# Kernel tuning notes

Hardware: AMD Instinct MI355X
Metric: run time of the kernel (lower is better)

Reference implementation:

```python
import jax, jax.numpy as jnp
import numpy as np

N_NODES = 100000
N_EDGES = 1600000
DIMS = [(2, 128), (128, 128), (128, 32), (32, 32), (32, 32)]


def setup_inputs() -> dict:
    key = jax.random.key(0)
    ks = jax.random.split(key, 2 + 3 * len(DIMS) + 2)
    x = jax.random.normal(ks[0], (N_NODES, 2), dtype=jnp.float32)
    edge_index = jax.random.randint(ks[1], (2, N_EDGES), 0, N_NODES, dtype=jnp.int32)
    inp = {"x": x, "edge_index": edge_index, "batch_size": 100}
    k = 2
    for i, (cin, cout) in enumerate(DIMS, start=1):
        s = 1.0 / np.sqrt(cin)
        inp[f"Wl{i}"] = jax.random.normal(ks[k], (cin, cout), dtype=jnp.float32) * s; k += 1
        inp[f"bl{i}"] = jnp.zeros((cout,), dtype=jnp.float32)
        inp[f"Wr{i}"] = jax.random.normal(ks[k], (cin, cout), dtype=jnp.float32) * s; k += 1
    inp["W_out"] = jax.random.normal(ks[k], (32, 1), dtype=jnp.float32) * (1.0 / np.sqrt(32.0)); k += 1
    inp["b_out"] = jnp.zeros((1,), dtype=jnp.float32)
    return inp


def reference(x, edge_index, batch_size,
              Wl1, bl1, Wr1, Wl2, bl2, Wr2, Wl3, bl3, Wr3,
              Wl4, bl4, Wr4, Wl5, bl5, Wr5, W_out, b_out):
    src, dst = edge_index[0], edge_index[1]
    h = x.reshape(-1, 2)
    n = h.shape[0]
    # in-degree per target node, clamped to 1 (PyG mean aggr gives 0 for isolated nodes)
    deg = jax.ops.segment_sum(jnp.ones_like(src, dtype=h.dtype), dst, num_segments=n)
    inv_deg = (1.0 / jnp.maximum(deg, 1.0))[:, None]

    def sage(h, Wl, bl, Wr):
        # mean-aggregate neighbor features, then SAGEConv: lin_l(agg) + lin_r(h)
        agg = jax.ops.segment_sum(h[src], dst, num_segments=n) * inv_deg
        return agg @ Wl + bl + h @ Wr

    for Wl, bl, Wr in ((Wl1, bl1, Wr1), (Wl2, bl2, Wr2), (Wl3, bl3, Wr3),
                       (Wl4, bl4, Wr4), (Wl5, bl5, Wr5)):
        h = jax.nn.relu(sage(h, Wl, bl, Wr))
    # dropout is identity in eval mode
    out = h @ W_out + b_out  # [n, 1]
    return out.reshape(batch_size, -1)
```

## Files before the change

### kernel.cpp

```cpp
#include <hip/hip_runtime.h>
#include <hip/hip_bf16.h>

#define N_NODES 100000
#define N_EDGES 1600000
#define NBUCK 256
#define NODES_PER_BUCKET 391
#define EDGES_PER_CHUNK (N_EDGES / NBUCK)
#define FILL_LDS_CAP 8192

typedef __bf16 bf16x8 __attribute__((ext_vector_type(8)));
typedef float f32x4 __attribute__((ext_vector_type(4)));


__device__ inline unsigned short f2bf_rne(float v) {
    unsigned u = __float_as_uint(v);
    u += 0x7fffu + ((u >> 16) & 1u);
    return (unsigned short)(u >> 16);
}

__device__ inline unsigned pack_bf(float a, float b) {
    return (unsigned)f2bf_rne(a) | ((unsigned)f2bf_rne(b) << 16);
}

__device__ inline void acc8_bf(float* a, uint4 p) {
    a[0] += __uint_as_float(p.x << 16);
    a[1] += __uint_as_float(p.x & 0xffff0000u);
    a[2] += __uint_as_float(p.y << 16);
    a[3] += __uint_as_float(p.y & 0xffff0000u);
    a[4] += __uint_as_float(p.z << 16);
    a[5] += __uint_as_float(p.z & 0xffff0000u);
    a[6] += __uint_as_float(p.w << 16);
    a[7] += __uint_as_float(p.w & 0xffff0000u);
}


__global__ __launch_bounds__(256) void pa_count(const int* __restrict__ dst,
                                                int* __restrict__ blkCntT) {
    __shared__ int hist[NBUCK];
    hist[threadIdx.x] = 0;
    __syncthreads();
    int b0 = blockIdx.x * EDGES_PER_CHUNK;
    int b1 = min(b0 + EDGES_PER_CHUNK, N_EDGES);
    for (int i = b0 + (int)threadIdx.x; i < b1; i += 256) {
        int d = __builtin_nontemporal_load(&dst[i]);
        atomicAdd(&hist[d / NODES_PER_BUCKET], 1);
    }
    __syncthreads();
    blkCntT[threadIdx.x * NBUCK + blockIdx.x] = hist[threadIdx.x];
}

__global__ __launch_bounds__(256) void pa_scan1(const int* __restrict__ blkCntT,
                                                int* __restrict__ blkBaseL,
                                                int* __restrict__ bucketTotal) {
    __shared__ int s[256];
    int t = threadIdx.x;
    int v = blkCntT[blockIdx.x * NBUCK + t];
    s[t] = v;
    __syncthreads();
    for (int off = 1; off < 256; off <<= 1) {
        int u = (t >= off) ? s[t - off] : 0;
        __syncthreads();
        s[t] += u;
        __syncthreads();
    }
    blkBaseL[blockIdx.x * NBUCK + t] = s[t] - v;
    if (t == 255) bucketTotal[blockIdx.x] = s[255];
}

__global__ __launch_bounds__(256) void pa_scan2(const int* __restrict__ bucketTotal,
                                                int* __restrict__ bstart,
                                                int* __restrict__ offsets) {
    __shared__ int s[256];
    int t = threadIdx.x;
    int v = bucketTotal[t];
    s[t] = v;
    __syncthreads();
    for (int off = 1; off < 256; off <<= 1) {
        int u = (t >= off) ? s[t - off] : 0;
        __syncthreads();
        s[t] += u;
        __syncthreads();
    }
    bstart[t] = s[t] - v;
    if (t == 255) {
        bstart[256] = s[255];
        offsets[N_NODES] = s[255];
    }
}

__global__ __launch_bounds__(256) void pa_scatter(const int* __restrict__ src,
                                                  const int* __restrict__ dst,
                                                  const int* __restrict__ blkBaseL,
                                                  const int* __restrict__ bstart,
                                                  int2* __restrict__ staging) {
    __shared__ int hist[NBUCK];
    __shared__ int runStart[NBUCK];
    __shared__ int cur[NBUCK];
    __shared__ int gbase[NBUCK];
    __shared__ int2 buf[EDGES_PER_CHUNK];

    const int tid = threadIdx.x;
    const int g = blockIdx.x;
    const int b0 = g * EDGES_PER_CHUNK;
    const int b1 = min(b0 + EDGES_PER_CHUNK, N_EDGES);

    hist[tid] = 0;
    __syncthreads();
    for (int i = b0 + tid; i < b1; i += 256) {
        int d = __builtin_nontemporal_load(&dst[i]);
        atomicAdd(&hist[d / NODES_PER_BUCKET], 1);
    }
    __syncthreads();
    {
        __shared__ int s[256];
        int v = hist[tid];
        s[tid] = v;
        __syncthreads();
        for (int off = 1; off < 256; off <<= 1) {
            int u = (tid >= off) ? s[tid - off] : 0;
            __syncthreads();
            s[tid] += u;
            __syncthreads();
        }
        runStart[tid] = s[tid] - v;
        cur[tid] = s[tid] - v;
        gbase[tid] = bstart[tid] + blkBaseL[tid * NBUCK + g];
    }
    __syncthreads();
    for (int i = b0 + tid; i < b1; i += 256) {
        int d = __builtin_nontemporal_load(&dst[i]);
        int s_ = __builtin_nontemporal_load(&src[i]);
        int k = d / NODES_PER_BUCKET;
        int p = atomicAdd(&cur[k], 1);
        buf[p] = make_int2(s_, d);
    }
    __syncthreads();
    int cnt = b1 - b0;
    for (int i = tid; i < cnt; i += 256) {
        int2 e = buf[i];
        int k = e.y / NODES_PER_BUCKET;
        staging[gbase[k] + (i - runStart[k])] = e;
    }
}

__global__ __launch_bounds__(512) void pc_fill(const int2* __restrict__ staging,
                                               const int* __restrict__ bstart,
                                               int* __restrict__ ssrc,
                                               int* __restrict__ offsets,
                                               float* __restrict__ inv_deg) {
    __shared__ int scnt[NODES_PER_BUCKET];
    __shared__ int sexc[NODES_PER_BUCKET];
    __shared__ int scur[NODES_PER_BUCKET];
    __shared__ int ssrcL[FILL_LDS_CAP];

    const int tid = threadIdx.x;
    const int b = blockIdx.x;
    const int node0 = b * NODES_PER_BUCKET;
    const int nn = min(node0 + NODES_PER_BUCKET, N_NODES) - node0;
    if (nn <= 0) return;
    const int es = bstart[b], ee = bstart[b + 1];
    const int cnt = ee - es;

    for (int j = tid; j < nn; j += 512) scnt[j] = 0;
    __syncthreads();
    for (int i = es + tid; i < ee; i += 512) {
        int2 e = staging[i];
        atomicAdd(&scnt[e.y - node0], 1);
    }
    __syncthreads();

    if (tid < 64) {
        int base = tid * 7;
        int vals[7];
        int run = 0;
#pragma unroll
        for (int j = 0; j < 7; ++j) {
            int idx = base + j;
            int c = (idx < nn) ? scnt[idx] : 0;
            vals[j] = run;
            run += c;
        }
        int inc = run;
#pragma unroll
        for (int off = 1; off < 64; off <<= 1) {
            int u = __shfl_up(inc, off, 64);
            if (tid >= off) inc += u;
        }
        int laneExcl = inc - run;
#pragma unroll
        for (int j = 0; j < 7; ++j) {
            int idx = base + j;
            if (idx < nn) sexc[idx] = laneExcl + vals[j];
        }
    }
    __syncthreads();

    for (int j = tid; j < nn; j += 512) {
        int c = scnt[j];
        int ex = sexc[j];
        offsets[node0 + j] = es + ex;
        inv_deg[node0 + j] = 1.0f / (float)max(c, 1);
        scur[j] = ex;
    }
    __syncthreads();

    if (cnt <= FILL_LDS_CAP) {
        for (int i = es + tid; i < ee; i += 512) {
            int2 e = staging[i];
            int p = atomicAdd(&scur[e.y - node0], 1);
            ssrcL[p] = e.x;
        }
        __syncthreads();
        for (int i = tid; i < cnt; i += 512) ssrc[es + i] = ssrcL[i];
    } else {
        for (int i = es + tid; i < ee; i += 512) {
            int2 e = staging[i];
            int p = atomicAdd(&scur[e.y - node0], 1);
            ssrc[es + p] = e.x;
        }
    }
}


__global__ __launch_bounds__(256) void aggregate_bf128(const unsigned short* __restrict__ hb,
                                                       const int* __restrict__ offs,
                                                       const int* __restrict__ ssrc,
                                                       const float* __restrict__ inv_deg,
                                                       unsigned short* __restrict__ aggb,
                                                       int nnodes) {
    int t = blockIdx.x * 256 + threadIdx.x;
    if (t >= nnodes * 16) return;
    int node = t >> 4;
    int c = t & 15;
    int b = offs[node], e = offs[node + 1];
    const uint4* __restrict__ hb4 = (const uint4*)hb;
    float acc[8] = {0.f, 0.f, 0.f, 0.f, 0.f, 0.f, 0.f, 0.f};
    int i = b;
    for (; i + 4 <= e; i += 4) {
        uint4 p0 = hb4[(size_t)ssrc[i] * 16 + c];
        uint4 p1 = hb4[(size_t)ssrc[i + 1] * 16 + c];
        uint4 p2 = hb4[(size_t)ssrc[i + 2] * 16 + c];
        uint4 p3 = hb4[(size_t)ssrc[i + 3] * 16 + c];
        acc8_bf(acc, p0);
        acc8_bf(acc, p1);
        acc8_bf(acc, p2);
        acc8_bf(acc, p3);
    }
    for (; i < e; ++i) {
        uint4 p = hb4[(size_t)ssrc[i] * 16 + c];
        acc8_bf(acc, p);
    }
    float s = inv_deg[node];
    uint4 o;
    o.x = pack_bf(acc[0] * s, acc[1] * s);
    o.y = pack_bf(acc[2] * s, acc[3] * s);
    o.z = pack_bf(acc[4] * s, acc[5] * s);
    o.w = pack_bf(acc[6] * s, acc[7] * s);
    ((uint4*)aggb)[t] = o;
}

__global__ __launch_bounds__(256) void aggregate_bf32(const unsigned short* __restrict__ hb,
                                                      const int* __restrict__ offs,
                                                      const int* __restrict__ ssrc,
                                                      const float* __restrict__ inv_deg,
                                                      float* __restrict__ agg, int nnodes) {
    int t = blockIdx.x * 256 + threadIdx.x;
    if (t >= nnodes * 4) return;
    int node = t >> 2;
    int c = t & 3;
    int b = offs[node], e = offs[node + 1];
    const uint4* __restrict__ hb4 = (const uint4*)hb;
    float acc[8] = {0.f, 0.f, 0.f, 0.f, 0.f, 0.f, 0.f, 0.f};
    int i = b;
    for (; i + 4 <= e; i += 4) {
        uint4 p0 = hb4[(size_t)ssrc[i] * 4 + c];
        uint4 p1 = hb4[(size_t)ssrc[i + 1] * 4 + c];
        uint4 p2 = hb4[(size_t)ssrc[i + 2] * 4 + c];
        uint4 p3 = hb4[(size_t)ssrc[i + 3] * 4 + c];
        acc8_bf(acc, p0);
        acc8_bf(acc, p1);
        acc8_bf(acc, p2);
        acc8_bf(acc, p3);
    }
    for (; i < e; ++i) {
        uint4 p = hb4[(size_t)ssrc[i] * 4 + c];
        acc8_bf(acc, p);
    }
    float s = inv_deg[node];
    float4* outp = (float4*)&agg[(size_t)node * 32 + c * 8];
    outp[0] = make_float4(acc[0] * s, acc[1] * s, acc[2] * s, acc[3] * s);
    outp[1] = make_float4(acc[4] * s, acc[5] * s, acc[6] * s, acc[7] * s);
}

__global__ __launch_bounds__(256) void aggregate2(const float* __restrict__ h,
                                                  const int* __restrict__ offs,
                                                  const int* __restrict__ ssrc,
                                                  const float* __restrict__ inv_deg,
                                                  float* __restrict__ agg, int nnodes) {
    int node = blockIdx.x * blockDim.x + threadIdx.x;
    if (node >= nnodes) return;
    int b = offs[node], e = offs[node + 1];
    const float2* __restrict__ h2 = (const float2*)h;
    float2 a0 = make_float2(0.f, 0.f), a1 = make_float2(0.f, 0.f);
    int i = b;
    for (; i + 2 <= e; i += 2) {
        float2 v = h2[ssrc[i]];
        float2 w = h2[ssrc[i + 1]];
        a0.x += v.x; a0.y += v.y;
        a1.x += w.x; a1.y += w.y;
    }
    if (i < e) {
        float2 v = h2[ssrc[i]];
        a0.x += v.x; a0.y += v.y;
    }
    float s = inv_deg[node];
    ((float2*)agg)[node] = make_float2((a0.x + a1.x) * s, (a0.y + a1.y) * s);
}


__global__ __launch_bounds__(256) void prep_wt(const float* __restrict__ Wl,
                                               const float* __restrict__ Wr,
                                               unsigned short* __restrict__ Wt) {
    int idx = blockIdx.x * 256 + threadIdx.x;
    int n = idx >> 8;
    int k = idx & 255;
    float v = (k < 128) ? Wl[k * 128 + n] : Wr[(k - 128) * 128 + n];
    Wt[idx] = f2bf_rne(v);
}

__global__ __launch_bounds__(256) void prep_w3(const float* __restrict__ Wl3,
                                               const float* __restrict__ Wr3,
                                               unsigned short* __restrict__ W3c) {
    int idx = blockIdx.x * 256 + threadIdx.x;
    if (idx >= 64 * 128) return;
    int n = idx >> 7;
    int k = idx & 127;
    float v = (n < 32) ? Wl3[k * 32 + n] : Wr3[k * 32 + (n - 32)];
    W3c[idx] = f2bf_rne(v);
}


__global__ __launch_bounds__(256) void gemm_l2_mfma(const unsigned short* __restrict__ Ab,
                                                    const unsigned short* __restrict__ Hb,
                                                    const unsigned short* __restrict__ Wt,
                                                    const float* __restrict__ bias,
                                                    const unsigned short* __restrict__ W3c,
                                                    unsigned short* __restrict__ g3b,
                                                    float* __restrict__ p3, int M) {
    constexpr int BM = 128, BK = 64;
    __shared__ unsigned short smem[26112];
#define SA(r, c) smem[(r) * 72 + (c)]
#define SB(r, c) smem[9216 + (r) * 72 + (c)]
#define SH(r, c) smem[(r) * 136 + (c)]
#define SW3(r, c) smem[17408 + (r) * 136 + (c)]

    const int tid = threadIdx.x;
    const int m0 = blockIdx.x * BM;
    const int lane = tid & 63;
    const int wid = tid >> 6;
    const int l15 = lane & 15;
    const int quad = lane >> 4;
    const int wm = (wid >> 1) * 64;
    const int wn = (wid & 1) * 64;

    f32x4 acc[4][4];
#pragma unroll
    for (int i = 0; i < 4; ++i)
#pragma unroll
        for (int j = 0; j < 4; ++j) acc[i][j] = (f32x4){0.f, 0.f, 0.f, 0.f};

    for (int k0 = 0; k0 < 256; k0 += BK) {
        const uint4* __restrict__ srcA = (const uint4*)((k0 < 128) ? Ab : Hb);
        const int kc = (k0 & 64) >> 3;
#pragma unroll
        for (int l = 0; l < 4; ++l) {
            int idx = tid + l * 256;
            int row = idx >> 3;
            int c8 = idx & 7;
            int gr = min(m0 + row, M - 1);
            uint4 va = srcA[(size_t)gr * 16 + kc + c8];
            *(uint4*)&SA(row, c8 * 8) = va;
            uint4 vb = ((const uint4*)Wt)[(size_t)row * 32 + (k0 >> 3) + c8];
            *(uint4*)&SB(row, c8 * 8) = vb;
        }
        __syncthreads();

#pragma unroll
        for (int ks = 0; ks < BK; ks += 32) {
            bf16x8 a[4], b[4];
#pragma unroll
            for (int t = 0; t < 4; ++t) {
                a[t] = *(const bf16x8*)&SA(wm + t * 16 + l15, ks + quad * 8);
                b[t] = *(const bf16x8*)&SB(wn + t * 16 + l15, ks + quad * 8);
            }
#pragma unroll
            for (int i = 0; i < 4; ++i)
#pragma unroll
                for (int j = 0; j < 4; ++j)
                    acc[i][j] = __builtin_amdgcn_mfma_f32_16x16x32_bf16(
                        a[i], b[j], acc[i][j], 0, 0, 0);
        }
        __syncthreads();
    }

#pragma unroll
    for (int j = 0; j < 4; ++j) {
        int n = wn + j * 16 + l15;
        float bv = bias[n];
#pragma unroll
        for (int i = 0; i < 4; ++i) {
#pragma unroll
            for (int r = 0; r < 4; ++r) {
                int ml = wm + i * 16 + quad * 4 + r;
                SH(ml, n) = f2bf_rne(fmaxf(acc[i][j][r] + bv, 0.f));
            }
        }
    }
#pragma unroll
    for (int l = 0; l < 4; ++l) {
        int idx = tid + l * 256;
        int row = idx >> 4;
        int c8 = idx & 15;
        uint4 v = ((const uint4*)W3c)[(size_t)row * 16 + c8];
        *(uint4*)&SW3(row, c8 * 8) = v;
    }
    __syncthreads();

    f32x4 acc2[2][4];
#pragma unroll
    for (int i = 0; i < 2; ++i)
#pragma unroll
        for (int j = 0; j < 4; ++j) acc2[i][j] = (f32x4){0.f, 0.f, 0.f, 0.f};

#pragma unroll
    for (int ks = 0; ks < 128; ks += 32) {
        bf16x8 a[2], b[4];
#pragma unroll
        for (int i = 0; i < 2; ++i)
            a[i] = *(const bf16x8*)&SH(wid * 32 + i * 16 + l15, ks + quad * 8);
#pragma unroll
        for (int j = 0; j < 4; ++j)
            b[j] = *(const bf16x8*)&SW3(j * 16 + l15, ks + quad * 8);
#pragma unroll
        for (int i = 0; i < 2; ++i)
#pragma unroll
            for (int j = 0; j < 4; ++j)
                acc2[i][j] = __builtin_amdgcn_mfma_f32_16x16x32_bf16(
                    a[i], b[j], acc2[i][j], 0, 0, 0);
    }

#pragma unroll
    for (int i = 0; i < 2; ++i) {
#pragma unroll
        for (int r = 0; r < 4; ++r) {
            int m = m0 + wid * 32 + i * 16 + quad * 4 + r;
            if (m >= M) continue;
#pragma unroll
            for (int j = 0; j < 4; ++j) {
                float v = acc2[i][j][r];
                if (j < 2) g3b[(size_t)m * 32 + j * 16 + l15] = f2bf_rne(v);
                else       p3[(size_t)m * 32 + (j - 2) * 16 + l15] = v;
            }
        }
    }
#undef SA
#undef SB
#undef SH
#undef SW3
}

__global__ __launch_bounds__(256) void combine3(const float* __restrict__ agg3,
                                                const float* __restrict__ p3,
                                                const float* __restrict__ bias,
                                                float* __restrict__ h3,
                                                unsigned short* __restrict__ h3b,
                                                int nnodes) {
    int idx = blockIdx.x * 256 + threadIdx.x;
    if (idx >= nnodes * 8) return;
    int c4 = idx & 7;
    float4 a = ((const float4*)agg3)[idx];
    float4 p = ((const float4*)p3)[idx];
    float4 bv = *(const float4*)&bias[c4 * 4];
    float4 r;
    r.x = fmaxf(a.x + p.x + bv.x, 0.f);
    r.y = fmaxf(a.y + p.y + bv.y, 0.f);
    r.z = fmaxf(a.z + p.z + bv.z, 0.f);
    r.w = fmaxf(a.w + p.w + bv.w, 0.f);
    ((float4*)h3)[idx] = r;
    uint2 o;
    o.x = pack_bf(r.x, r.y);
    o.y = pack_bf(r.z, r.w);
    ((uint2*)h3b)[idx] = o;
}


template <int Cin, bool EMIT_BF, bool FUSE_OUT>
__global__ __launch_bounds__(256) void gemm_n32(const float* __restrict__ A0,
                                                const float* __restrict__ A1,
                                                const float* __restrict__ W0,
                                                const float* __restrict__ bias,
                                                const float* __restrict__ W1,
                                                float* __restrict__ C,
                                                unsigned short* __restrict__ Cbf,
                                                const float* __restrict__ Wout,
                                                const float* __restrict__ bout,
                                                float* __restrict__ out, int M) {
    constexpr int COUT = 32, BM = 128, BK = 16;
    __shared__ float sA0[BK][BM + 4];
    __shared__ float sA1[BK][BM + 4];
    __shared__ float sW0[BK][36];
    __shared__ float sW1[BK][36];

    const int tid = threadIdx.x;
    const int m0 = blockIdx.x * BM;
    const int tr = tid >> 3;
    const int tc = tid & 7;

    float acc[4][4];
#pragma unroll
    for (int i = 0; i < 4; ++i)
#pragma unroll
        for (int j = 0; j < 4; ++j) acc[i][j] = 0.f;

    const int wrow = tid >> 3;
    const int wc4  = tid & 7;

    for (int k0 = 0; k0 < Cin; k0 += BK) {
#pragma unroll
        for (int l = 0; l < 2; ++l) {
            int idx = tid + l * 256;
            int row = idx >> 2;
            int c4  = idx & 3;
            int gr  = min(m0 + row, M - 1);
            float4 v0 = *(const float4*)&A0[(size_t)gr * Cin + k0 + c4 * 4];
            float4 v1 = *(const float4*)&A1[(size_t)gr * Cin + k0 + c4 * 4];
            sA0[c4 * 4 + 0][row] = v0.x; sA0[c4 * 4 + 1][row] = v0.y;
            sA0[c4 * 4 + 2][row] = v0.z; sA0[c4 * 4 + 3][row] = v0.w;
            sA1[c4 * 4 + 0][row] = v1.x; sA1[c4 * 4 + 1][row] = v1.y;
            sA1[c4 * 4 + 2][row] = v1.z; sA1[c4 * 4 + 3][row] = v1.w;
        }
        if (tid < 128) {
            float4 w0 = *(const float4*)&W0[(size_t)(k0 + wrow) * COUT + wc4 * 4];
            float4 w1 = *(const float4*)&W1[(size_t)(k0 + wrow) * COUT + wc4 * 4];
            *(float4*)&sW0[wrow][wc4 * 4] = w0;
            *(float4*)&sW1[wrow][wc4 * 4] = w1;
        }
        __syncthreads();

#pragma unroll
        for (int k = 0; k < BK; ++k) {
            float4 a0 = *(const float4*)&sA0[k][tr * 4];
            float4 a1 = *(const float4*)&sA1[k][tr * 4];
            float4 w0 = *(const float4*)&sW0[k][tc * 4];
            float4 w1 = *(const float4*)&sW1[k][tc * 4];
            float av0[4] = {a0.x, a0.y, a0.z, a0.w};
            float av1[4] = {a1.x, a1.y, a1.z, a1.w};
            float wv0[4] = {w0.x, w0.y, w0.z, w0.w};
            float wv1[4] = {w1.x, w1.y, w1.z, w1.w};
#pragma unroll
            for (int i = 0; i < 4; ++i)
#pragma unroll
                for (int j = 0; j < 4; ++j)
                    acc[i][j] = fmaf(av0[i], wv0[j], fmaf(av1[i], wv1[j], acc[i][j]));
        }
        __syncthreads();
    }

#pragma unroll
    for (int i = 0; i < 4; ++i) {
        int m = m0 + tr * 4 + i;
        if (m >= M) continue;
        int n = tc * 4;
        float4 bv = *(const float4*)&bias[n];
        float4 r;
        r.x = fmaxf(acc[i][0] + bv.x, 0.f);
        r.y = fmaxf(acc[i][1] + bv.y, 0.f);
        r.z = fmaxf(acc[i][2] + bv.z, 0.f);
        r.w = fmaxf(acc[i][3] + bv.w, 0.f);
        if (FUSE_OUT) {
            float p = r.x * Wout[n] + r.y * Wout[n + 1] +
                      r.z * Wout[n + 2] + r.w * Wout[n + 3];
            p += __shfl_down(p, 4, 8);
            p += __shfl_down(p, 2, 8);
            p += __shfl_down(p, 1, 8);
            if (tc == 0) out[m] = p + bout[0];
        } else {
            *(float4*)&C[(size_t)m * COUT + n] = r;
            if (EMIT_BF) {
                uint2 o;
                o.x = pack_bf(r.x, r.y);
                o.y = pack_bf(r.z, r.w);
                *(uint2*)&Cbf[(size_t)m * COUT + n] = o;
            }
        }
    }
}

__global__ __launch_bounds__(256) void sage_linear2(const float* __restrict__ agg,
                                                    const float* __restrict__ h,
                                                    const float* __restrict__ Wl,
                                                    const float* __restrict__ bl,
                                                    const float* __restrict__ Wr,
                                                    unsigned short* __restrict__ out_bf,
                                                    int nnodes) {
    constexpr int Cout = 128;
    int t = blockIdx.x * blockDim.x + threadIdx.x;
    if (t >= nnodes * Cout) return;
    int node = t / Cout;
    int c = t - node * Cout;
    float2 a = ((const float2*)agg)[node];
    float2 hh = ((const float2*)h)[node];
    float acc = bl[c];
    acc = fmaf(a.x, Wl[c], acc);
    acc = fmaf(a.y, Wl[Cout + c], acc);
    acc = fmaf(hh.x, Wr[c], acc);
    acc = fmaf(hh.y, Wr[Cout + c], acc);
    acc = fmaxf(acc, 0.f);
    out_bf[t] = f2bf_rne(acc);
}


extern "C" void kernel_launch(void* const* d_in, const int* in_sizes, int n_in,
                              void* d_out, int out_size, void* d_ws, size_t ws_size,
                              hipStream_t stream) {
    const float* x      = (const float*)d_in[0];
    const int*   ei     = (const int*)d_in[1];
    const float* Wl1    = (const float*)d_in[3];
    const float* bl1    = (const float*)d_in[4];
    const float* Wr1    = (const float*)d_in[5];
    const float* Wl2    = (const float*)d_in[6];
    const float* bl2    = (const float*)d_in[7];
    const float* Wr2    = (const float*)d_in[8];
    const float* Wl3    = (const float*)d_in[9];
    const float* bl3    = (const float*)d_in[10];
    const float* Wr3    = (const float*)d_in[11];
    const float* Wl4    = (const float*)d_in[12];
    const float* bl4    = (const float*)d_in[13];
    const float* Wr4    = (const float*)d_in[14];
    const float* Wl5    = (const float*)d_in[15];
    const float* bl5    = (const float*)d_in[16];
    const float* Wr5    = (const float*)d_in[17];
    const float* W_out  = (const float*)d_in[18];
    const float* b_out  = (const float*)d_in[19];
    float* out = (float*)d_out;

    const int N = N_NODES, E = N_EDGES;
    const int* e_src = ei;
    const int* e_dst = ei + E;

    size_t off = 0;
    auto carve = [&](size_t bytes) {
        void* p = (char*)d_ws + off;
        off += (bytes + 255) & ~(size_t)255;
        return p;
    };
    int*   offsets  = (int*)carve((size_t)(N + 1) * 4);
    float* inv_deg  = (float*)carve((size_t)N * 4);
    int*   ssrc     = (int*)carve((size_t)E * 4);
    int*   blkCntT  = (int*)carve((size_t)NBUCK * NBUCK * 4);
    int*   blkBaseL = (int*)carve((size_t)NBUCK * NBUCK * 4);
    int*   bucketTotal = (int*)carve((size_t)NBUCK * 4);
    int*   bstart   = (int*)carve((size_t)(NBUCK + 1) * 4);
    int2*  staging  = (int2*)carve((size_t)E * 8);
    unsigned short* Wt  = (unsigned short*)carve((size_t)128 * 256 * 2);
    unsigned short* W3c = (unsigned short*)carve((size_t)64 * 128 * 2);
    float* agg      = (float*)carve((size_t)N * 128 * 4);
    float* bufA     = (float*)carve((size_t)N * 128 * 4);
    unsigned short* g3b = (unsigned short*)carve((size_t)N * 32 * 2);
    unsigned short* h3b = (unsigned short*)carve((size_t)N * 32 * 2);
    unsigned short* h4b = (unsigned short*)carve((size_t)N * 32 * 2);

    float* slotA = agg;
    float* slotB = agg + (size_t)N * 32;
    float* slotC = agg + (size_t)N * 64;
    float* slotD = agg + (size_t)N * 96;
    unsigned short* h1_bf = (unsigned short*)bufA;
    unsigned short* aggB  = (unsigned short*)bufA + (size_t)N * 128;

    pa_count<<<NBUCK, 256, 0, stream>>>(e_dst, blkCntT);
    pa_scan1<<<NBUCK, 256, 0, stream>>>(blkCntT, blkBaseL, bucketTotal);
    pa_scan2<<<1, 256, 0, stream>>>(bucketTotal, bstart, offsets);
    pa_scatter<<<NBUCK, 256, 0, stream>>>(e_src, e_dst, blkBaseL, bstart, staging);
    pc_fill<<<NBUCK, 512, 0, stream>>>(staging, bstart, ssrc, offsets, inv_deg);
    prep_wt<<<128, 256, 0, stream>>>(Wl2, Wr2, Wt);
    prep_w3<<<32, 256, 0, stream>>>(Wl3, Wr3, W3c);

    const int gemm_grid = (N + 127) / 128;

    aggregate2<<<(N + 255) / 256, 256, 0, stream>>>(x, offsets, ssrc, inv_deg, slotC, N);
    sage_linear2<<<(N * 128 + 255) / 256, 256, 0, stream>>>(slotC, x, Wl1, bl1, Wr1, h1_bf, N);

    aggregate_bf128<<<(N * 16 + 255) / 256, 256, 0, stream>>>(h1_bf, offsets, ssrc,
                                                              inv_deg, aggB, N);
    gemm_l2_mfma<<<gemm_grid, 256, 0, stream>>>(aggB, h1_bf, Wt, bl2, W3c, g3b, slotA, N);

    aggregate_bf32<<<(N * 4 + 255) / 256, 256, 0, stream>>>(g3b, offsets, ssrc, inv_deg, slotB, N);
    combine3<<<(N * 8 + 255) / 256, 256, 0, stream>>>(slotB, slotA, bl3, slotC, h3b, N);

    aggregate_bf32<<<(N * 4 + 255) / 256, 256, 0, stream>>>(h3b, offsets, ssrc, inv_deg, slotD, N);
    gemm_n32<32, true, false><<<gemm_grid, 256, 0, stream>>>(slotD, slotC, Wl4, bl4, Wr4,
                                                             slotA, h4b, nullptr, nullptr,
                                                             nullptr, N);

    aggregate_bf32<<<(N * 4 + 255) / 256, 256, 0, stream>>>(h4b, offsets, ssrc, inv_deg, slotB, N);
    gemm_n32<32, false, true><<<gemm_grid, 256, 0, stream>>>(slotB, slotA, Wl5, bl5, Wr5,
                                                             nullptr, nullptr, W_out, b_out,
                                                             out, N);
}
```

Measured before the change: 377.4 us.

## Project-then-aggregate for layers 4-5 with MFMA combine kernels and reuse histograms

Layers 4 and 5 now apply the linear projection before aggregation: a combine kernel adds bias and ReLU to the previous layer, then uses bf16 MFMA to compute both the lin_l projection (stored as bf16 for gathering) and the lin_r projection (kept in fp32). The final layer is a small per-node kernel that fuses bias, ReLU and the output dot product. The fp32 h3/h4 intermediates and the separate combine and fp32 GEMM kernels go away, which cuts launches and memory traffic. pa_scatter also reuses the per-block histograms already computed by pa_count instead of re-reading dst and rebuilding them with atomics. In exchange, the MFMA inputs for layers 4 and 5 are rounded to bf16, which adds precision error.

After: 372.5 us. No clear change (-1.3%).

```diff
diff --git a/kernel.cpp b/kernel.cpp
--- a/kernel.cpp
+++ b/kernel.cpp
@@ -90,10 +90,10 @@
 
 __global__ __launch_bounds__(256) void pa_scatter(const int* __restrict__ src,
                                                   const int* __restrict__ dst,
+                                                  const int* __restrict__ blkCntT,
                                                   const int* __restrict__ blkBaseL,
                                                   const int* __restrict__ bstart,
                                                   int2* __restrict__ staging) {
-    __shared__ int hist[NBUCK];
     __shared__ int runStart[NBUCK];
     __shared__ int cur[NBUCK];
     __shared__ int gbase[NBUCK];
@@ -104,16 +104,9 @@
     const int b0 = g * EDGES_PER_CHUNK;
     const int b1 = min(b0 + EDGES_PER_CHUNK, N_EDGES);
 
-    hist[tid] = 0;
-    __syncthreads();
-    for (int i = b0 + tid; i < b1; i += 256) {
-        int d = __builtin_nontemporal_load(&dst[i]);
-        atomicAdd(&hist[d / NODES_PER_BUCKET], 1);
-    }
-    __syncthreads();
     {
         __shared__ int s[256];
-        int v = hist[tid];
+        int v = blkCntT[tid * NBUCK + g];
         s[tid] = v;
         __syncthreads();
         for (int off = 1; off < 256; off <<= 1) {
@@ -339,6 +332,17 @@
     W3c[idx] = f2bf_rne(v);
 }
 
+__global__ __launch_bounds__(256) void prep_w32(const float* __restrict__ Wl,
+                                                const float* __restrict__ Wr,
+                                                unsigned short* __restrict__ Wc) {
+    int idx = blockIdx.x * 256 + threadIdx.x;
+    if (idx >= 64 * 32) return;
+    int n = idx >> 5;
+    int k = idx & 31;
+    float v = (n < 32) ? Wl[k * 32 + n] : Wr[k * 32 + (n - 32)];
+    Wc[idx] = f2bf_rne(v);
+}
+
 
 __global__ __launch_bounds__(256) void gemm_l2_mfma(const unsigned short* __restrict__ Ab,
                                                     const unsigned short* __restrict__ Hb,
@@ -469,131 +473,101 @@
 #undef SW3
 }
 
-__global__ __launch_bounds__(256) void combine3(const float* __restrict__ agg3,
-                                                const float* __restrict__ p3,
-                                                const float* __restrict__ bias,
-                                                float* __restrict__ h3,
-                                                unsigned short* __restrict__ h3b,
-                                                int nnodes) {
-    int idx = blockIdx.x * 256 + threadIdx.x;
-    if (idx >= nnodes * 8) return;
-    int c4 = idx & 7;
-    float4 a = ((const float4*)agg3)[idx];
-    float4 p = ((const float4*)p3)[idx];
-    float4 bv = *(const float4*)&bias[c4 * 4];
-    float4 r;
-    r.x = fmaxf(a.x + p.x + bv.x, 0.f);
-    r.y = fmaxf(a.y + p.y + bv.y, 0.f);
-    r.z = fmaxf(a.z + p.z + bv.z, 0.f);
-    r.w = fmaxf(a.w + p.w + bv.w, 0.f);
-    ((float4*)h3)[idx] = r;
-    uint2 o;
-    o.x = pack_bf(r.x, r.y);
-    o.y = pack_bf(r.z, r.w);
-    ((uint2*)h3b)[idx] = o;
-}
-
-
-template <int Cin, bool EMIT_BF, bool FUSE_OUT>
-__global__ __launch_bounds__(256) void gemm_n32(const float* __restrict__ A0,
-                                                const float* __restrict__ A1,
-                                                const float* __restrict__ W0,
-                                                const float* __restrict__ bias,
-                                                const float* __restrict__ W1,
-                                                float* __restrict__ C,
-                                                unsigned short* __restrict__ Cbf,
-                                                const float* __restrict__ Wout,
-                                                const float* __restrict__ bout,
-                                                float* __restrict__ out, int M) {
-    constexpr int COUT = 32, BM = 128, BK = 16;
-    __shared__ float sA0[BK][BM + 4];
-    __shared__ float sA1[BK][BM + 4];
-    __shared__ float sW0[BK][36];
-    __shared__ float sW1[BK][36];
+
+__global__ __launch_bounds__(256) void combine_mfma(const float* __restrict__ agg,
+                                                    const float* __restrict__ p,
+                                                    const float* __restrict__ bias,
+                                                    const unsigned short* __restrict__ Wc,
+                                                    unsigned short* __restrict__ gb,
+                                                    float* __restrict__ pnext, int M) {
+    __shared__ unsigned short sH[128][40];
+    __shared__ unsigned short sW[64][40];
 
     const int tid = threadIdx.x;
-    const int m0 = blockIdx.x * BM;
-    const int tr = tid >> 3;
-    const int tc = tid & 7;
-
-    float acc[4][4];
-#pragma unroll
-    for (int i = 0; i < 4; ++i)
-#pragma unroll
-        for (int j = 0; j < 4; ++j) acc[i][j] = 0.f;
-
-    const int wrow = tid >> 3;
-    const int wc4  = tid & 7;
-
-    for (int k0 = 0; k0 < Cin; k0 += BK) {
-#pragma unroll
-        for (int l = 0; l < 2; ++l) {
-            int idx = tid + l * 256;
-            int row = idx >> 2;
-            int c4  = idx & 3;
-            int gr  = min(m0 + row, M - 1);
-            float4 v0 = *(const float4*)&A0[(size_t)gr * Cin + k0 + c4 * 4];
-            float4 v1 = *(const float4*)&A1[(size_t)gr * Cin + k0 + c4 * 4];
-            sA0[c4 * 4 + 0][row] = v0.x; sA0[c4 * 4 + 1][row] = v0.y;
-            sA0[c4 * 4 + 2][row] = v0.z; sA0[c4 * 4 + 3][row] = v0.w;
-            sA1[c4 * 4 + 0][row] = v1.x; sA1[c4 * 4 + 1][row] = v1.y;
-            sA1[c4 * 4 + 2][row] = v1.z; sA1[c4 * 4 + 3][row] = v1.w;
-        }
-        if (tid < 128) {
-            float4 w0 = *(const float4*)&W0[(size_t)(k0 + wrow) * COUT + wc4 * 4];
-            float4 w1 = *(const float4*)&W1[(size_t)(k0 + wrow) * COUT + wc4 * 4];
-            *(float4*)&sW0[wrow][wc4 * 4] = w0;
-            *(float4*)&sW1[wrow][wc4 * 4] = w1;
-        }
-        __syncthreads();
-
-#pragma unroll
-        for (int k = 0; k < BK; ++k) {
-            float4 a0 = *(const float4*)&sA0[k][tr * 4];
-            float4 a1 = *(const float4*)&sA1[k][tr * 4];
-            float4 w0 = *(const float4*)&sW0[k][tc * 4];
-            float4 w1 = *(const float4*)&sW1[k][tc * 4];
-            float av0[4] = {a0.x, a0.y, a0.z, a0.w};
-            float av1[4] = {a1.x, a1.y, a1.z, a1.w};
-            float wv0[4] = {w0.x, w0.y, w0.z, w0.w};
-            float wv1[4] = {w1.x, w1.y, w1.z, w1.w};
-#pragma unroll
-            for (int i = 0; i < 4; ++i)
-#pragma unroll
-                for (int j = 0; j < 4; ++j)
-                    acc[i][j] = fmaf(av0[i], wv0[j], fmaf(av1[i], wv1[j], acc[i][j]));
-        }
-        __syncthreads();
-    }
-
-#pragma unroll
-    for (int i = 0; i < 4; ++i) {
-        int m = m0 + tr * 4 + i;
-        if (m >= M) continue;
-        int n = tc * 4;
-        float4 bv = *(const float4*)&bias[n];
-        float4 r;
-        r.x = fmaxf(acc[i][0] + bv.x, 0.f);
-        r.y = fmaxf(acc[i][1] + bv.y, 0.f);
-        r.z = fmaxf(acc[i][2] + bv.z, 0.f);
-        r.w = fmaxf(acc[i][3] + bv.w, 0.f);
-        if (FUSE_OUT) {
-            float p = r.x * Wout[n] + r.y * Wout[n + 1] +
-                      r.z * Wout[n + 2] + r.w * Wout[n + 3];
-            p += __shfl_down(p, 4, 8);
-            p += __shfl_down(p, 2, 8);
-            p += __shfl_down(p, 1, 8);
-            if (tc == 0) out[m] = p + bout[0];
-        } else {
-            *(float4*)&C[(size_t)m * COUT + n] = r;
-            if (EMIT_BF) {
-                uint2 o;
-                o.x = pack_bf(r.x, r.y);
-                o.y = pack_bf(r.z, r.w);
-                *(uint2*)&Cbf[(size_t)m * COUT + n] = o;
+    const int m0 = blockIdx.x * 128;
+    const int lane = tid & 63;
+    const int wid = tid >> 6;
+    const int l15 = lane & 15;
+    const int quad = lane >> 4;
+
+#pragma unroll
+    for (int l = 0; l < 4; ++l) {
+        int idx = tid + l * 256;
+        int row = idx >> 3;
+        int c4 = idx & 7;
+        int gr = min(m0 + row, M - 1);
+        float4 a = *(const float4*)&agg[(size_t)gr * 32 + c4 * 4];
+        float4 pv = *(const float4*)&p[(size_t)gr * 32 + c4 * 4];
+        float4 bv = *(const float4*)&bias[c4 * 4];
+        uint2 o;
+        o.x = pack_bf(fmaxf(a.x + pv.x + bv.x, 0.f), fmaxf(a.y + pv.y + bv.y, 0.f));
+        o.y = pack_bf(fmaxf(a.z + pv.z + bv.z, 0.f), fmaxf(a.w + pv.w + bv.w, 0.f));
+        *(uint2*)&sH[row][c4 * 4] = o;
+    }
+#pragma unroll
+    for (int l = 0; l < 2; ++l) {
+        int idx = tid + l * 256;
+        int row = idx >> 3;
+        int c4 = idx & 7;
+        uint2 v = ((const uint2*)Wc)[(size_t)row * 8 + c4];
+        *(uint2*)&sW[row][c4 * 4] = v;
+    }
+    __syncthreads();
+
+    f32x4 acc[2][4];
+    bf16x8 a[2], b[4];
+#pragma unroll
+    for (int i = 0; i < 2; ++i)
+        a[i] = *(const bf16x8*)&sH[wid * 32 + i * 16 + l15][quad * 8];
+#pragma unroll
+    for (int j = 0; j < 4; ++j)
+        b[j] = *(const bf16x8*)&sW[j * 16 + l15][quad * 8];
+#pragma unroll
+    for (int i = 0; i < 2; ++i)
+#pragma unroll
+        for (int j = 0; j < 4; ++j)
+            acc[i][j] = __builtin_amdgcn_mfma_f32_16x16x32_bf16(
+                a[i], b[j], (f32x4){0.f, 0.f, 0.f, 0.f}, 0, 0, 0);
+
+#pragma unroll
+    for (int i = 0; i < 2; ++i) {
+#pragma unroll
+        for (int r = 0; r < 4; ++r) {
+            int m = m0 + wid * 32 + i * 16 + quad * 4 + r;
+            if (m >= M) continue;
+#pragma unroll
+            for (int j = 0; j < 4; ++j) {
+                float v = acc[i][j][r];
+                if (j < 2) gb[(size_t)m * 32 + j * 16 + l15] = f2bf_rne(v);
+                else       pnext[(size_t)m * 32 + (j - 2) * 16 + l15] = v;
             }
         }
     }
+}
+
+__global__ __launch_bounds__(256) void final5(const float* __restrict__ agg,
+                                              const float* __restrict__ p,
+                                              const float* __restrict__ bias,
+                                              const float* __restrict__ Wout,
+                                              const float* __restrict__ bout,
+                                              float* __restrict__ out, int nnodes) {
+    int n = blockIdx.x * 256 + threadIdx.x;
+    if (n >= nnodes) return;
+    const float4* a4 = (const float4*)(agg + (size_t)n * 32);
+    const float4* p4 = (const float4*)(p + (size_t)n * 32);
+    float acc = bout[0];
+#pragma unroll
+    for (int k4 = 0; k4 < 8; ++k4) {
+        float4 a = a4[k4];
+        float4 pv = p4[k4];
+        const float* bv = bias + k4 * 4;
+        const float* w = Wout + k4 * 4;
+        acc = fmaf(fmaxf(a.x + pv.x + bv[0], 0.f), w[0], acc);
+        acc = fmaf(fmaxf(a.y + pv.y + bv[1], 0.f), w[1], acc);
+        acc = fmaf(fmaxf(a.z + pv.z + bv[2], 0.f), w[2], acc);
+        acc = fmaf(fmaxf(a.w + pv.w + bv[3], 0.f), w[3], acc);
+    }
+    out[n] = acc;
 }
 
 __global__ __launch_bounds__(256) void sage_linear2(const float* __restrict__ agg,
@@ -664,11 +638,13 @@
     int2*  staging  = (int2*)carve((size_t)E * 8);
     unsigned short* Wt  = (unsigned short*)carve((size_t)128 * 256 * 2);
     unsigned short* W3c = (unsigned short*)carve((size_t)64 * 128 * 2);
+    unsigned short* W4c = (unsigned short*)carve((size_t)64 * 32 * 2);
+    unsigned short* W5c = (unsigned short*)carve((size_t)64 * 32 * 2);
     float* agg      = (float*)carve((size_t)N * 128 * 4);
     float* bufA     = (float*)carve((size_t)N * 128 * 4);
     unsigned short* g3b = (unsigned short*)carve((size_t)N * 32 * 2);
-    unsigned short* h3b = (unsigned short*)carve((size_t)N * 32 * 2);
-    unsigned short* h4b = (unsigned short*)carve((size_t)N * 32 * 2);
+    unsigned short* g4b = (unsigned short*)carve((size_t)N * 32 * 2);
+    unsigned short* g5b = (unsigned short*)carve((size_t)N * 32 * 2);
 
     float* slotA = agg;
     float* slotB = agg + (size_t)N * 32;
@@ -680,10 +656,12 @@
     pa_count<<<NBUCK, 256, 0, stream>>>(e_dst, blkCntT);
     pa_scan1<<<NBUCK, 256, 0, stream>>>(blkCntT, blkBaseL, bucketTotal);
     pa_scan2<<<1, 256, 0, stream>>>(bucketTotal, bstart, offsets);
-    pa_scatter<<<NBUCK, 256, 0, stream>>>(e_src, e_dst, blkBaseL, bstart, staging);
+    pa_scatter<<<NBUCK, 256, 0, stream>>>(e_src, e_dst, blkCntT, blkBaseL, bstart, staging);
     pc_fill<<<NBUCK, 512, 0, stream>>>(staging, bstart, ssrc, offsets, inv_deg);
     prep_wt<<<128, 256, 0, stream>>>(Wl2, Wr2, Wt);
     prep_w3<<<32, 256, 0, stream>>>(Wl3, Wr3, W3c);
+    prep_w32<<<8, 256, 0, stream>>>(Wl4, Wr4, W4c);
+    prep_w32<<<8, 256, 0, stream>>>(Wl5, Wr5, W5c);
 
     const int gemm_grid = (N + 127) / 128;
 
@@ -695,15 +673,11 @@
     gemm_l2_mfma<<<gemm_grid, 256, 0, stream>>>(aggB, h1_bf, Wt, bl2, W3c, g3b, slotA, N);
 
     aggregate_bf32<<<(N * 4 + 255) / 256, 256, 0, stream>>>(g3b, offsets, ssrc, inv_deg, slotB, N);
-    combine3<<<(N * 8 + 255) / 256, 256, 0, stream>>>(slotB, slotA, bl3, slotC, h3b, N);
-
-    aggregate_bf32<<<(N * 4 + 255) / 256, 256, 0, stream>>>(h3b, offsets, ssrc, inv_deg, slotD, N);
-    gemm_n32<32, true, false><<<gemm_grid, 256, 0, stream>>>(slotD, slotC, Wl4, bl4, Wr4,
-                                                             slotA, h4b, nullptr, nullptr,
-                                                             nullptr, N);
-
-    aggregate_bf32<<<(N * 4 + 255) / 256, 256, 0, stream>>>(h4b, offsets, ssrc, inv_deg, slotB, N);
-    gemm_n32<32, false, true><<<gemm_grid, 256, 0, stream>>>(slotB, slotA, Wl5, bl5, Wr5,
-                                                             nullptr, nullptr, W_out, b_out,
-                                                             out, N);
-}
+    combine_mfma<<<gemm_grid, 256, 0, stream>>>(slotB, slotA, bl3, W4c, g4b, slotC, N);
+
+    aggregate_bf32<<<(N * 4 + 255) / 256, 256, 0, stream>>>(g4b, offsets, ssrc, inv_deg, slotD, N);
+    combine_mfma<<<gemm_grid, 256, 0, stream>>>(slotD, slotC, bl4, W5c, g5b, slotA, N);
+
+    aggregate_bf32<<<(N * 4 + 255) / 256, 256, 0, stream>>>(g5b, offsets, ssrc, inv_deg, slotB, N);
+    final5<<<(N + 255) / 256, 256, 0, stream>>>(slotB, slotA, bl5, W_out, b_out, out, N);
+}
```
